# Kernel tuning notes

Measured on AMD Instinct MI355X. Metric: run time of the kernel, lower is better.

Reference implementation:

```python
import jax, jax.numpy as jnp
import numpy as np

B, N, C, H = 2, 2048, 1024, 16
D = C // H  # head_dim = 64


def _rope_freqs(n, d_half, theta=10000.0):
    inv = 1.0 / (theta ** (np.arange(0, d_half, dtype=np.float32) / d_half))
    ang = np.arange(n, dtype=np.float32)[:, None] * inv[None, :]
    return jnp.asarray(np.cos(ang)), jnp.asarray(np.sin(ang))


def setup_inputs() -> dict:
    key = jax.random.key(0)
    ks = jax.random.split(key, 5)
    cos, sin = _rope_freqs(N, D // 2)
    s = 0.02
    return {
        "x": jax.random.normal(ks[0], (B, N, C), jnp.float32),
        "w_qkv": jax.random.normal(ks[1], (3 * C, C), jnp.float32) * s,
        "b_qkv": jnp.zeros((3 * C,), jnp.float32),
        "w_proj": jax.random.normal(ks[2], (C, C), jnp.float32) * s,
        "b_proj": jnp.zeros((C,), jnp.float32),
        "freqs_cos": cos,
        "freqs_sin": sin,
    }


def _apply_rope(t, cos, sin):
    # t: (B, H, N, D); consecutive pairs (even, odd) form complex numbers,
    # matching torch.view_as_complex on reshape(..., D//2, 2).
    te = t[..., 0::2]
    to = t[..., 1::2]
    cos = cos[None, None, :, :]  # (1,1,N,D//2)
    sin = sin[None, None, :, :]
    oe = te * cos - to * sin
    oo = te * sin + to * cos
    return jnp.stack([oe, oo], axis=-1).reshape(t.shape)


def reference(x, w_qkv, b_qkv, w_proj, b_proj, freqs_cos, freqs_sin):
    b, n, c = x.shape
    qkv = x @ w_qkv.T + b_qkv                      # (B,N,3C)
    qkv = qkv.reshape(b, n, 3, H, D).transpose(2, 0, 3, 1, 4)  # (3,B,H,N,D)
    q, k, v = qkv[0], qkv[1], qkv[2]
    q = _apply_rope(q, freqs_cos, freqs_sin)
    k = _apply_rope(k, freqs_cos, freqs_sin)
    scale = 1.0 / jnp.sqrt(jnp.asarray(D, x.dtype))
    scores = jnp.einsum("bhqd,bhkd->bhqk", q, k) * scale
    attn = jax.nn.softmax(scores, axis=-1)
    out = jnp.einsum("bhqk,bhkd->bhqd", attn, v)   # (B,H,N,D)
    out = out.transpose(0, 2, 1, 3).reshape(b, n, c)
    return out @ w_proj.T + b_proj
```

## Files before the change

### kernel.cpp

```cpp
#include <hip/hip_runtime.h>
#include <hip/hip_bf16.h>
#include <stdint.h>

#define BB 2
#define NN 2048
#define CC 1024
#define HH 16
#define DD 64
#define C3 3072

typedef __attribute__((ext_vector_type(8))) short bf16x8;
typedef __attribute__((ext_vector_type(4))) float f32x4;
typedef __attribute__((ext_vector_type(4))) unsigned short ushort4_t;

__device__ __forceinline__ unsigned short f2bf(float f) {
  union { float f; unsigned u; } v; v.f = f;
  unsigned r = v.u + 0x7FFFu + ((v.u >> 16) & 1u);
  return (unsigned short)(r >> 16);
}

#if __has_builtin(__builtin_amdgcn_exp2f)
#define EXP2(x) __builtin_amdgcn_exp2f(x)
#else
#define EXP2(x) exp2f(x)
#endif

#define QSCALE 0.18033688f

#define GLDS(g, l) __builtin_amdgcn_global_load_lds( \
    (const __attribute__((address_space(1))) void*)(g), \
    (__attribute__((address_space(3))) void*)(l), 16, 0, 0)

__global__ __launch_bounds__(256) void k_cvt(
    const float* __restrict__ x, const float* __restrict__ wq,
    const float* __restrict__ wp,
    unsigned short* __restrict__ xb, unsigned short* __restrict__ wqb,
    unsigned short* __restrict__ wpb)
{
  int blk = blockIdx.x;
  const float* s; unsigned short* d; int i;
  if (blk < 4096)      { s = x;  d = xb;  i = blk * 256 + threadIdx.x; }
  else if (blk < 7168) { s = wq; d = wqb; i = (blk - 4096) * 256 + threadIdx.x; }
  else                 { s = wp; d = wpb; i = (blk - 7168) * 256 + threadIdx.x; }
  float4 v = ((const float4*)s)[i];
  ushort4_t o;
  o.x = f2bf(v.x); o.y = f2bf(v.y); o.z = f2bf(v.z); o.w = f2bf(v.w);
  ((ushort4_t*)d)[i] = o;
}

__global__ __launch_bounds__(256) void k_gemm_qkv(
    const unsigned short* __restrict__ A, const unsigned short* __restrict__ Bt,
    const float* __restrict__ bias,
    const float* __restrict__ cosb, const float* __restrict__ sinb,
    unsigned short* __restrict__ Qg, unsigned short* __restrict__ Kg,
    unsigned short* __restrict__ Vnd)
{
  __shared__ __align__(16) unsigned short As[128 * 32];
  __shared__ __align__(16) unsigned short Bs[128 * 32];
  const int tid  = threadIdx.x;
  const int lane = tid & 63;
  const int wave = tid >> 6;
  const int bm = blockIdx.y * 128;
  const int bn = blockIdx.x * 128;
  const int wm = (wave >> 1) * 64;
  const int wn = (wave & 1) * 64;
  const int frow = lane & 15;
  const int fk   = (lane >> 4) * 8;
  const int K = 1024;

  f32x4 acc[4][4] = {};

  const int row0 = tid >> 2, cc0 = tid & 3;
  const int row1 = row0 + 64;

  for (int k0 = 0; k0 < K; k0 += 32) {
    GLDS(A  + (size_t)(bm + row0) * K + k0 + cc0 * 8, As + (size_t)tid * 8);
    GLDS(Bt + (size_t)(bn + row0) * K + k0 + cc0 * 8, Bs + (size_t)tid * 8);
    GLDS(A  + (size_t)(bm + row1) * K + k0 + cc0 * 8, As + (size_t)(tid + 256) * 8);
    GLDS(Bt + (size_t)(bn + row1) * K + k0 + cc0 * 8, Bs + (size_t)(tid + 256) * 8);
    __syncthreads();

    bf16x8 af[4], bfr[4];
#pragma unroll
    for (int t = 0; t < 4; ++t) {
      af[t]  = *(const bf16x8*)(As + (wm + t * 16 + frow) * 32 + fk);
      bfr[t] = *(const bf16x8*)(Bs + (wn + t * 16 + frow) * 32 + fk);
    }
#pragma unroll
    for (int mt = 0; mt < 4; ++mt)
#pragma unroll
      for (int nt = 0; nt < 4; ++nt)
        acc[mt][nt] = __builtin_amdgcn_mfma_f32_16x16x32_bf16(af[mt], bfr[nt], acc[mt][nt], 0, 0, 0);
    __syncthreads();
  }

  const int er0  = (lane >> 4) * 4;
  const int ecol = lane & 15;
  const int region = bn >> 10;
  unsigned short* dstQK = (region == 0) ? Qg : Kg;

#pragma unroll
  for (int nt = 0; nt < 4; ++nt) {
    const int col = bn + wn + nt * 16 + ecol;
    const float bv = bias[col];
    const int c64 = (wn + nt * 16 + ecol) & 63;
    const int h   = (col >> 6) & 15;
    const int ii  = c64 >> 1;
#pragma unroll
    for (int mt = 0; mt < 4; ++mt)
#pragma unroll
      for (int r = 0; r < 4; ++r) {
        const int rowg = bm + wm + mt * 16 + er0 + r;
        const int b = rowg >> 11, n = rowg & (NN - 1);
        float v = acc[mt][nt][r] + bv;
        float vp = __shfl_xor(v, 1, 64);
        const size_t o = ((size_t)(b * HH + h) * NN + n) * DD + c64;
        if (region == 2) {
          Vnd[o] = f2bf(v);
        } else {
          float cth = cosb[n * 32 + ii], sth = sinb[n * 32 + ii];
          float ov = (c64 & 1) ? (vp * sth + v * cth)
                               : (v * cth - vp * sth);
          if (region == 0) ov *= QSCALE;
          dstQK[o] = f2bf(ov);
        }
      }
  }
}

__global__ __launch_bounds__(256) void k_vt(
    const unsigned short* __restrict__ Vnd, unsigned short* __restrict__ Vt)
{
  __shared__ unsigned short t[64][66];
  const int tid = threadIdx.x;
  const int bh = blockIdx.x >> 5;
  const int n0 = (blockIdx.x & 31) * 64;

  const unsigned short* src = Vnd + ((size_t)bh * NN + n0) * DD;
  const int nl = tid >> 2, d0 = (tid & 3) * 16;
#pragma unroll
  for (int j = 0; j < 4; ++j) {
    ushort4_t v = *(const ushort4_t*)(src + (size_t)nl * DD + d0 + j * 4);
    t[nl][d0 + j * 4 + 0] = v.x;
    t[nl][d0 + j * 4 + 1] = v.y;
    t[nl][d0 + j * 4 + 2] = v.z;
    t[nl][d0 + j * 4 + 3] = v.w;
  }
  __syncthreads();
  const int d = tid >> 2, m0 = (tid & 3) * 16;
  unsigned short* dst = Vt + ((size_t)bh * DD + d) * NN + n0 + m0;
#pragma unroll
  for (int j = 0; j < 4; ++j) {
    ushort4_t o;
    o.x = t[m0 + j * 4 + 0][d];
    o.y = t[m0 + j * 4 + 1][d];
    o.z = t[m0 + j * 4 + 2][d];
    o.w = t[m0 + j * 4 + 3][d];
    *(ushort4_t*)(dst + j * 4) = o;
  }
}

__global__ __launch_bounds__(256) void k_attn(
    const unsigned short* __restrict__ Qg, const unsigned short* __restrict__ Kg,
    const unsigned short* __restrict__ Vtg, unsigned short* __restrict__ Og)
{
  __shared__ __align__(16) unsigned short Ks[2][64 * 64];
  __shared__ __align__(16) unsigned short Vs[2][64 * 64];
  __shared__ __align__(16) unsigned short Ps[4][32 * 64];

  const int tid  = threadIdx.x;
  const int lane = tid & 63;
  const int wave = tid >> 6;
  const int bh = blockIdx.x >> 4;
  const int qt = blockIdx.x & 15;
  const int q0 = qt * 128 + wave * 32;
  const int frow   = lane & 15;
  const int fchunk = lane >> 4;
  const int er0  = (lane >> 4) * 4;
  const int ecol = lane & 15;

  const unsigned short* Qb = Qg  + (size_t)bh * NN * DD;
  const unsigned short* Kb = Kg  + (size_t)bh * NN * DD;
  const unsigned short* Vb = Vtg + (size_t)bh * DD * NN;

  bf16x8 qf[2][2];
#pragma unroll
  for (int m = 0; m < 2; ++m)
#pragma unroll
    for (int kt = 0; kt < 2; ++kt)
      qf[m][kt] = *(const bf16x8*)(Qb + (size_t)(q0 + m * 16 + frow) * DD + kt * 32 + fchunk * 8);

  bf16x8 ones;
#pragma unroll
  for (int i = 0; i < 8; ++i) ones[i] = (short)0x3F80;

  f32x4 oacc[2][4] = {};
  f32x4 lacc[2] = {};

  const int row0 = tid >> 3, cc0 = tid & 7;
  const int sw0 = (cc0 ^ (row0 & 7)) * 8;

  GLDS(Kb + (size_t)row0 * DD + sw0,        Ks[0] + (size_t)tid * 8);
  GLDS(Vb + (size_t)row0 * NN + sw0,        Vs[0] + (size_t)tid * 8);
  GLDS(Kb + (size_t)(row0 + 32) * DD + sw0, Ks[0] + (size_t)(tid + 256) * 8);
  GLDS(Vb + (size_t)(row0 + 32) * NN + sw0, Vs[0] + (size_t)(tid + 256) * 8);

  for (int t = 0; t < NN / 64; ++t) {
    const int p = t & 1;
    __syncthreads();

    if (t + 1 < NN / 64) {
      const int j = (t + 1) * 64;
      GLDS(Kb + (size_t)(j + row0) * DD + sw0,      Ks[1 - p] + (size_t)tid * 8);
      GLDS(Vb + (size_t)row0 * NN + j + sw0,        Vs[1 - p] + (size_t)tid * 8);
      GLDS(Kb + (size_t)(j + row0 + 32) * DD + sw0, Ks[1 - p] + (size_t)(tid + 256) * 8);
      GLDS(Vb + (size_t)(row0 + 32) * NN + j + sw0, Vs[1 - p] + (size_t)(tid + 256) * 8);
    }

    f32x4 sacc[2][4] = {};
#pragma unroll
    for (int nt = 0; nt < 4; ++nt) {
      int kr = nt * 16 + frow;
      bf16x8 kf0 = *(const bf16x8*)(Ks[p] + kr * 64 + ((fchunk       ^ (kr & 7)) << 3));
      bf16x8 kf1 = *(const bf16x8*)(Ks[p] + kr * 64 + (((fchunk + 4) ^ (kr & 7)) << 3));
#pragma unroll
      for (int m = 0; m < 2; ++m) {
        sacc[m][nt] = __builtin_amdgcn_mfma_f32_16x16x32_bf16(qf[m][0], kf0, sacc[m][nt], 0, 0, 0);
        sacc[m][nt] = __builtin_amdgcn_mfma_f32_16x16x32_bf16(qf[m][1], kf1, sacc[m][nt], 0, 0, 0);
      }
    }

#pragma unroll
    for (int m = 0; m < 2; ++m)
#pragma unroll
      for (int r = 0; r < 4; ++r) {
        int prow = m * 16 + er0 + r;
#pragma unroll
        for (int nt = 0; nt < 4; ++nt) {
          float pv = EXP2(sacc[m][nt][r]);
          union { float f; unsigned u; } cv; cv.f = pv;
          int col = nt * 16 + ecol;
          Ps[wave][prow * 64 + (((col >> 3) ^ (prow & 7)) << 3) + (col & 7)] =
              (unsigned short)(cv.u >> 16);
        }
      }

    bf16x8 pf0[2], pf1[2];
#pragma unroll
    for (int m = 0; m < 2; ++m) {
      int pr = m * 16 + frow;
      pf0[m] = *(const bf16x8*)(&Ps[wave][pr * 64 + ((fchunk       ^ (pr & 7)) << 3)]);
      pf1[m] = *(const bf16x8*)(&Ps[wave][pr * 64 + (((fchunk + 4) ^ (pr & 7)) << 3)]);
      lacc[m] = __builtin_amdgcn_mfma_f32_16x16x32_bf16(pf0[m], ones, lacc[m], 0, 0, 0);
      lacc[m] = __builtin_amdgcn_mfma_f32_16x16x32_bf16(pf1[m], ones, lacc[m], 0, 0, 0);
    }
#pragma unroll
    for (int dt = 0; dt < 4; ++dt) {
      int vr = dt * 16 + frow;
      bf16x8 vf0 = *(const bf16x8*)(Vs[p] + vr * 64 + ((fchunk       ^ (vr & 7)) << 3));
      bf16x8 vf1 = *(const bf16x8*)(Vs[p] + vr * 64 + (((fchunk + 4) ^ (vr & 7)) << 3));
#pragma unroll
      for (int m = 0; m < 2; ++m) {
        oacc[m][dt] = __builtin_amdgcn_mfma_f32_16x16x32_bf16(pf0[m], vf0, oacc[m][dt], 0, 0, 0);
        oacc[m][dt] = __builtin_amdgcn_mfma_f32_16x16x32_bf16(pf1[m], vf1, oacc[m][dt], 0, 0, 0);
      }
    }
  }

  const int b = bh >> 4;
  const int h = bh & 15;
#pragma unroll
  for (int m = 0; m < 2; ++m)
#pragma unroll
    for (int dt = 0; dt < 4; ++dt)
#pragma unroll
      for (int r = 0; r < 4; ++r) {
        int qrow = q0 + m * 16 + er0 + r;
        int d = dt * 16 + ecol;
        float v = oacc[m][dt][r] / lacc[m][r];
        Og[(size_t)(b * NN + qrow) * CC + h * DD + d] = f2bf(v);
      }
}

__global__ __launch_bounds__(256) void k_gemm_proj(
    const unsigned short* __restrict__ A, const unsigned short* __restrict__ Bt,
    const float* __restrict__ bias, float* __restrict__ Co)
{
  __shared__ __align__(16) unsigned short As[64 * 32];
  __shared__ __align__(16) unsigned short Bs[128 * 32];
  const int tid  = threadIdx.x;
  const int lane = tid & 63;
  const int wave = tid >> 6;
  const int bm = blockIdx.y * 64;
  const int bn = blockIdx.x * 128;
  const int wm = (wave >> 1) * 32;
  const int wn = (wave & 1) * 64;
  const int frow = lane & 15;
  const int fk   = (lane >> 4) * 8;
  const int K = 1024;

  f32x4 acc[2][4] = {};

  const int row0 = tid >> 2, cc0 = tid & 3;

  for (int k0 = 0; k0 < K; k0 += 32) {
    GLDS(A  + (size_t)(bm + row0) * K + k0 + cc0 * 8, As + (size_t)tid * 8);
    GLDS(Bt + (size_t)(bn + row0) * K + k0 + cc0 * 8, Bs + (size_t)tid * 8);
    GLDS(Bt + (size_t)(bn + row0 + 64) * K + k0 + cc0 * 8, Bs + (size_t)(tid + 256) * 8);
    __syncthreads();

    bf16x8 af[2], bfr[4];
#pragma unroll
    for (int t = 0; t < 2; ++t)
      af[t] = *(const bf16x8*)(As + (wm + t * 16 + frow) * 32 + fk);
#pragma unroll
    for (int t = 0; t < 4; ++t)
      bfr[t] = *(const bf16x8*)(Bs + (wn + t * 16 + frow) * 32 + fk);
#pragma unroll
    for (int mt = 0; mt < 2; ++mt)
#pragma unroll
      for (int nt = 0; nt < 4; ++nt)
        acc[mt][nt] = __builtin_amdgcn_mfma_f32_16x16x32_bf16(af[mt], bfr[nt], acc[mt][nt], 0, 0, 0);
    __syncthreads();
  }

  const int er0  = (lane >> 4) * 4;
  const int ecol = lane & 15;
#pragma unroll
  for (int nt = 0; nt < 4; ++nt) {
    int col = bn + wn + nt * 16 + ecol;
    float bv = bias[col];
#pragma unroll
    for (int mt = 0; mt < 2; ++mt)
#pragma unroll
      for (int r = 0; r < 4; ++r) {
        int rowg = bm + wm + mt * 16 + er0 + r;
        Co[(size_t)rowg * CC + col] = acc[mt][nt][r] + bv;
      }
  }
}

extern "C" void kernel_launch(void* const* d_in, const int* in_sizes, int n_in,
                              void* d_out, int out_size, void* d_ws, size_t ws_size,
                              hipStream_t stream)
{
  const float* x      = (const float*)d_in[0];
  const float* w_qkv  = (const float*)d_in[1];
  const float* b_qkv  = (const float*)d_in[2];
  const float* w_proj = (const float*)d_in[3];
  const float* b_proj = (const float*)d_in[4];
  const float* fcos   = (const float*)d_in[5];
  const float* fsin   = (const float*)d_in[6];
  float* out = (float*)d_out;

  char* ws = (char*)d_ws;
  unsigned short* xb     = (unsigned short*)(ws);
  unsigned short* wqkvb  = (unsigned short*)(ws + 8388608);
  unsigned short* wprojb = (unsigned short*)(ws + 14680064);
  unsigned short* Qb     = (unsigned short*)(ws + 16777216);
  unsigned short* Kb     = (unsigned short*)(ws + 25165824);
  unsigned short* Vnd    = (unsigned short*)(ws + 33554432);
  unsigned short* Vtb    = (unsigned short*)(ws + 41943040);
  unsigned short* aob    = (unsigned short*)(ws + 50331648);

  k_cvt<<<8192, 256, 0, stream>>>(x, w_qkv, w_proj, xb, wqkvb, wprojb);

  k_gemm_qkv<<<dim3(24, 32), 256, 0, stream>>>(xb, wqkvb, b_qkv, fcos, fsin,
                                               Qb, Kb, Vnd);
  k_vt<<<1024, 256, 0, stream>>>(Vnd, Vtb);

  k_attn<<<512, 256, 0, stream>>>(Qb, Kb, Vtb, aob);

  k_gemm_proj<<<dim3(8, 64), 256, 0, stream>>>(aob, wprojb, b_proj, out);
}
```

Measured before the change: 226.5 us.

## Split attention over key halves with combine kernel; widen GEMM K-tiles with swizzle

Attention is split across two halves of the key sequence, doubling the block count from 512 to 1024 to fill more compute units. Each half writes unnormalized fp32 partial outputs and row sums, and a new combine kernel adds them, normalizes and emits bf16. Both GEMMs now stage 64-wide K tiles with an XOR-swizzled LDS layout, halving the number of barrier iterations and avoiding bank conflicts. The split adds a kernel launch and about 33 MB of extra fp32 global traffic. Skipping max-subtraction is safe only because partials combine linearly.

```diff
diff --git a/kernel.cpp b/kernel.cpp
--- a/kernel.cpp
+++ b/kernel.cpp
@@ -55,8 +55,8 @@
     unsigned short* __restrict__ Qg, unsigned short* __restrict__ Kg,
     unsigned short* __restrict__ Vnd)
 {
-  __shared__ __align__(16) unsigned short As[128 * 32];
-  __shared__ __align__(16) unsigned short Bs[128 * 32];
+  __shared__ __align__(16) unsigned short As[128 * 64];
+  __shared__ __align__(16) unsigned short Bs[128 * 64];
   const int tid  = threadIdx.x;
   const int lane = tid & 63;
   const int wave = tid >> 6;
@@ -64,33 +64,41 @@
   const int bn = blockIdx.x * 128;
   const int wm = (wave >> 1) * 64;
   const int wn = (wave & 1) * 64;
-  const int frow = lane & 15;
-  const int fk   = (lane >> 4) * 8;
+  const int frow   = lane & 15;
+  const int fchunk = lane >> 4;
   const int K = 1024;
 
   f32x4 acc[4][4] = {};
 
-  const int row0 = tid >> 2, cc0 = tid & 3;
-  const int row1 = row0 + 64;
-
-  for (int k0 = 0; k0 < K; k0 += 32) {
-    GLDS(A  + (size_t)(bm + row0) * K + k0 + cc0 * 8, As + (size_t)tid * 8);
-    GLDS(Bt + (size_t)(bn + row0) * K + k0 + cc0 * 8, Bs + (size_t)tid * 8);
-    GLDS(A  + (size_t)(bm + row1) * K + k0 + cc0 * 8, As + (size_t)(tid + 256) * 8);
-    GLDS(Bt + (size_t)(bn + row1) * K + k0 + cc0 * 8, Bs + (size_t)(tid + 256) * 8);
+  const int srow[4] = { tid >> 3, 32 + (tid >> 3), 64 + (tid >> 3), 96 + (tid >> 3) };
+  int scol[4];
+#pragma unroll
+  for (int j = 0; j < 4; ++j) scol[j] = ((tid & 7) ^ (srow[j] & 7)) * 8;
+
+  for (int k0 = 0; k0 < K; k0 += 64) {
+#pragma unroll
+    for (int j = 0; j < 4; ++j) {
+      GLDS(A  + (size_t)(bm + srow[j]) * K + k0 + scol[j], As + (size_t)(j * 256 + tid) * 8);
+      GLDS(Bt + (size_t)(bn + srow[j]) * K + k0 + scol[j], Bs + (size_t)(j * 256 + tid) * 8);
+    }
     __syncthreads();
 
-    bf16x8 af[4], bfr[4];
-#pragma unroll
-    for (int t = 0; t < 4; ++t) {
-      af[t]  = *(const bf16x8*)(As + (wm + t * 16 + frow) * 32 + fk);
-      bfr[t] = *(const bf16x8*)(Bs + (wn + t * 16 + frow) * 32 + fk);
-    }
-#pragma unroll
-    for (int mt = 0; mt < 4; ++mt)
-#pragma unroll
-      for (int nt = 0; nt < 4; ++nt)
-        acc[mt][nt] = __builtin_amdgcn_mfma_f32_16x16x32_bf16(af[mt], bfr[nt], acc[mt][nt], 0, 0, 0);
+#pragma unroll
+    for (int kh = 0; kh < 2; ++kh) {
+      bf16x8 af[4], bfr[4];
+#pragma unroll
+      for (int t = 0; t < 4; ++t) {
+        int ra = wm + t * 16 + frow;
+        int rb = wn + t * 16 + frow;
+        af[t]  = *(const bf16x8*)(As + ra * 64 + (((kh * 4 + fchunk) ^ (ra & 7)) << 3));
+        bfr[t] = *(const bf16x8*)(Bs + rb * 64 + (((kh * 4 + fchunk) ^ (rb & 7)) << 3));
+      }
+#pragma unroll
+      for (int mt = 0; mt < 4; ++mt)
+#pragma unroll
+        for (int nt = 0; nt < 4; ++nt)
+          acc[mt][nt] = __builtin_amdgcn_mfma_f32_16x16x32_bf16(af[mt], bfr[nt], acc[mt][nt], 0, 0, 0);
+    }
     __syncthreads();
   }
 
@@ -162,17 +170,20 @@
 
 __global__ __launch_bounds__(256) void k_attn(
     const unsigned short* __restrict__ Qg, const unsigned short* __restrict__ Kg,
-    const unsigned short* __restrict__ Vtg, unsigned short* __restrict__ Og)
+    const unsigned short* __restrict__ Vtg,
+    float* __restrict__ Op, float* __restrict__ lp)
 {
   __shared__ __align__(16) unsigned short Ks[2][64 * 64];
   __shared__ __align__(16) unsigned short Vs[2][64 * 64];
-  __shared__ __align__(16) unsigned short Ps[4][32 * 64];
+  __shared__ __align__(16) unsigned short Ps[4][32 * 32];
 
   const int tid  = threadIdx.x;
   const int lane = tid & 63;
   const int wave = tid >> 6;
-  const int bh = blockIdx.x >> 4;
-  const int qt = blockIdx.x & 15;
+  const int blk  = blockIdx.x;
+  const int bh   = blk >> 5;
+  const int qt   = (blk >> 1) & 15;
+  const int half = blk & 1;
   const int q0 = qt * 128 + wave * 32;
   const int frow   = lane & 15;
   const int fchunk = lane >> 4;
@@ -182,6 +193,7 @@
   const unsigned short* Qb = Qg  + (size_t)bh * NN * DD;
   const unsigned short* Kb = Kg  + (size_t)bh * NN * DD;
   const unsigned short* Vb = Vtg + (size_t)bh * DD * NN;
+  const int jbase = half * (NN / 2);
 
   bf16x8 qf[2][2];
 #pragma unroll
@@ -200,17 +212,17 @@
   const int row0 = tid >> 3, cc0 = tid & 7;
   const int sw0 = (cc0 ^ (row0 & 7)) * 8;
 
-  GLDS(Kb + (size_t)row0 * DD + sw0,        Ks[0] + (size_t)tid * 8);
-  GLDS(Vb + (size_t)row0 * NN + sw0,        Vs[0] + (size_t)tid * 8);
-  GLDS(Kb + (size_t)(row0 + 32) * DD + sw0, Ks[0] + (size_t)(tid + 256) * 8);
-  GLDS(Vb + (size_t)(row0 + 32) * NN + sw0, Vs[0] + (size_t)(tid + 256) * 8);
-
-  for (int t = 0; t < NN / 64; ++t) {
+  GLDS(Kb + (size_t)(jbase + row0) * DD + sw0,      Ks[0] + (size_t)tid * 8);
+  GLDS(Vb + (size_t)row0 * NN + jbase + sw0,        Vs[0] + (size_t)tid * 8);
+  GLDS(Kb + (size_t)(jbase + row0 + 32) * DD + sw0, Ks[0] + (size_t)(tid + 256) * 8);
+  GLDS(Vb + (size_t)(row0 + 32) * NN + jbase + sw0, Vs[0] + (size_t)(tid + 256) * 8);
+
+  for (int t = 0; t < NN / 128; ++t) {
     const int p = t & 1;
     __syncthreads();
 
-    if (t + 1 < NN / 64) {
-      const int j = (t + 1) * 64;
+    if (t + 1 < NN / 128) {
+      const int j = jbase + (t + 1) * 64;
       GLDS(Kb + (size_t)(j + row0) * DD + sw0,      Ks[1 - p] + (size_t)tid * 8);
       GLDS(Vb + (size_t)row0 * NN + j + sw0,        Vs[1 - p] + (size_t)tid * 8);
       GLDS(Kb + (size_t)(j + row0 + 32) * DD + sw0, Ks[1 - p] + (size_t)(tid + 256) * 8);
@@ -231,63 +243,87 @@
     }
 
 #pragma unroll
-    for (int m = 0; m < 2; ++m)
-#pragma unroll
-      for (int r = 0; r < 4; ++r) {
-        int prow = m * 16 + er0 + r;
-#pragma unroll
-        for (int nt = 0; nt < 4; ++nt) {
-          float pv = EXP2(sacc[m][nt][r]);
-          union { float f; unsigned u; } cv; cv.f = pv;
-          int col = nt * 16 + ecol;
-          Ps[wave][prow * 64 + (((col >> 3) ^ (prow & 7)) << 3) + (col & 7)] =
-              (unsigned short)(cv.u >> 16);
+    for (int kh = 0; kh < 2; ++kh) {
+#pragma unroll
+      for (int m = 0; m < 2; ++m)
+#pragma unroll
+        for (int r = 0; r < 4; ++r) {
+          int prow = m * 16 + er0 + r;
+#pragma unroll
+          for (int nh = 0; nh < 2; ++nh) {
+            float pv = EXP2(sacc[m][kh * 2 + nh][r]);
+            union { float f; unsigned u; } cv; cv.f = pv;
+            int cl = nh * 16 + ecol;
+            Ps[wave][prow * 32 + (((cl >> 3) ^ (prow & 3)) << 3) + (cl & 7)] =
+                (unsigned short)(cv.u >> 16);
+          }
         }
-      }
-
-    bf16x8 pf0[2], pf1[2];
-#pragma unroll
-    for (int m = 0; m < 2; ++m) {
-      int pr = m * 16 + frow;
-      pf0[m] = *(const bf16x8*)(&Ps[wave][pr * 64 + ((fchunk       ^ (pr & 7)) << 3)]);
-      pf1[m] = *(const bf16x8*)(&Ps[wave][pr * 64 + (((fchunk + 4) ^ (pr & 7)) << 3)]);
-      lacc[m] = __builtin_amdgcn_mfma_f32_16x16x32_bf16(pf0[m], ones, lacc[m], 0, 0, 0);
-      lacc[m] = __builtin_amdgcn_mfma_f32_16x16x32_bf16(pf1[m], ones, lacc[m], 0, 0, 0);
-    }
-#pragma unroll
-    for (int dt = 0; dt < 4; ++dt) {
-      int vr = dt * 16 + frow;
-      bf16x8 vf0 = *(const bf16x8*)(Vs[p] + vr * 64 + ((fchunk       ^ (vr & 7)) << 3));
-      bf16x8 vf1 = *(const bf16x8*)(Vs[p] + vr * 64 + (((fchunk + 4) ^ (vr & 7)) << 3));
+
+      bf16x8 pf[2];
 #pragma unroll
       for (int m = 0; m < 2; ++m) {
-        oacc[m][dt] = __builtin_amdgcn_mfma_f32_16x16x32_bf16(pf0[m], vf0, oacc[m][dt], 0, 0, 0);
-        oacc[m][dt] = __builtin_amdgcn_mfma_f32_16x16x32_bf16(pf1[m], vf1, oacc[m][dt], 0, 0, 0);
-      }
-    }
-  }
-
-  const int b = bh >> 4;
-  const int h = bh & 15;
-#pragma unroll
-  for (int m = 0; m < 2; ++m)
+        int pr = m * 16 + frow;
+        pf[m] = *(const bf16x8*)(&Ps[wave][pr * 32 + ((fchunk ^ (pr & 3)) << 3)]);
+        lacc[m] = __builtin_amdgcn_mfma_f32_16x16x32_bf16(pf[m], ones, lacc[m], 0, 0, 0);
+      }
+#pragma unroll
+      for (int dt = 0; dt < 4; ++dt) {
+        int vr = dt * 16 + frow;
+        bf16x8 vf = *(const bf16x8*)(Vs[p] + vr * 64 + (((kh * 4 + fchunk) ^ (vr & 7)) << 3));
+#pragma unroll
+        for (int m = 0; m < 2; ++m)
+          oacc[m][dt] = __builtin_amdgcn_mfma_f32_16x16x32_bf16(pf[m], vf, oacc[m][dt], 0, 0, 0);
+      }
+    }
+  }
+
+  float* Oh = Op + (size_t)half * (32u * NN * DD);
+#pragma unroll
+  for (int m = 0; m < 2; ++m) {
 #pragma unroll
     for (int dt = 0; dt < 4; ++dt)
 #pragma unroll
       for (int r = 0; r < 4; ++r) {
         int qrow = q0 + m * 16 + er0 + r;
         int d = dt * 16 + ecol;
-        float v = oacc[m][dt][r] / lacc[m][r];
-        Og[(size_t)(b * NN + qrow) * CC + h * DD + d] = f2bf(v);
-      }
+        Oh[((size_t)bh * NN + qrow) * DD + d] = oacc[m][dt][r];
+      }
+    if (ecol == 0) {
+#pragma unroll
+      for (int r = 0; r < 4; ++r) {
+        int qrow = q0 + m * 16 + er0 + r;
+        lp[(size_t)half * (32 * NN) + bh * NN + qrow] = lacc[m][r];
+      }
+    }
+  }
+}
+
+__global__ __launch_bounds__(256) void k_combine(
+    const float* __restrict__ Op, const float* __restrict__ lp,
+    unsigned short* __restrict__ aob)
+{
+  int idx = blockIdx.x * 256 + threadIdx.x;
+  int q  = idx >> 4;
+  int d4 = (idx & 15) * 4;
+  const float4 a = *(const float4*)(Op + (size_t)q * DD + d4);
+  const float4 b = *(const float4*)(Op + (size_t)(32u * NN * DD) + (size_t)q * DD + d4);
+  float inv = 1.0f / (lp[q] + lp[32 * NN + q]);
+  int bh = q >> 11, n = q & (NN - 1);
+  int bb = bh >> 4, h = bh & 15;
+  ushort4_t o;
+  o.x = f2bf((a.x + b.x) * inv);
+  o.y = f2bf((a.y + b.y) * inv);
+  o.z = f2bf((a.z + b.z) * inv);
+  o.w = f2bf((a.w + b.w) * inv);
+  *(ushort4_t*)(aob + ((size_t)(bb * NN + n) * CC) + h * DD + d4) = o;
 }
 
 __global__ __launch_bounds__(256) void k_gemm_proj(
     const unsigned short* __restrict__ A, const unsigned short* __restrict__ Bt,
     const float* __restrict__ bias, float* __restrict__ Co)
 {
-  __shared__ __align__(16) unsigned short As[64 * 32];
-  __shared__ __align__(16) unsigned short Bs[128 * 32];
+  __shared__ __align__(16) unsigned short As[64 * 64];
+  __shared__ __align__(16) unsigned short Bs[128 * 64];
   const int tid  = threadIdx.x;
   const int lane = tid & 63;
   const int wave = tid >> 6;
@@ -295,32 +331,47 @@
   const int bn = blockIdx.x * 128;
   const int wm = (wave >> 1) * 32;
   const int wn = (wave & 1) * 64;
-  const int frow = lane & 15;
-  const int fk   = (lane >> 4) * 8;
+  const int frow   = lane & 15;
+  const int fchunk = lane >> 4;
   const int K = 1024;
 
   f32x4 acc[2][4] = {};
 
-  const int row0 = tid >> 2, cc0 = tid & 3;
-
-  for (int k0 = 0; k0 < K; k0 += 32) {
-    GLDS(A  + (size_t)(bm + row0) * K + k0 + cc0 * 8, As + (size_t)tid * 8);
-    GLDS(Bt + (size_t)(bn + row0) * K + k0 + cc0 * 8, Bs + (size_t)tid * 8);
-    GLDS(Bt + (size_t)(bn + row0 + 64) * K + k0 + cc0 * 8, Bs + (size_t)(tid + 256) * 8);
+  const int r0 = tid >> 3;
+  const int sc0 = ((tid & 7) ^ (r0 & 7)) * 8;
+  const int r1 = 32 + r0;
+  const int sc1 = ((tid & 7) ^ (r1 & 7)) * 8;
+
+  for (int k0 = 0; k0 < K; k0 += 64) {
+    GLDS(A + (size_t)(bm + r0) * K + k0 + sc0, As + (size_t)tid * 8);
+    GLDS(A + (size_t)(bm + r1) * K + k0 + sc1, As + (size_t)(tid + 256) * 8);
+#pragma unroll
+    for (int j = 0; j < 4; ++j) {
+      int rb = j * 32 + r0;
+      int scb = ((tid & 7) ^ (rb & 7)) * 8;
+      GLDS(Bt + (size_t)(bn + rb) * K + k0 + scb, Bs + (size_t)(j * 256 + tid) * 8);
+    }
     __syncthreads();
 
-    bf16x8 af[2], bfr[4];
-#pragma unroll
-    for (int t = 0; t < 2; ++t)
-      af[t] = *(const bf16x8*)(As + (wm + t * 16 + frow) * 32 + fk);
-#pragma unroll
-    for (int t = 0; t < 4; ++t)
-      bfr[t] = *(const bf16x8*)(Bs + (wn + t * 16 + frow) * 32 + fk);
-#pragma unroll
-    for (int mt = 0; mt < 2; ++mt)
-#pragma unroll
-      for (int nt = 0; nt < 4; ++nt)
-        acc[mt][nt] = __builtin_amdgcn_mfma_f32_16x16x32_bf16(af[mt], bfr[nt], acc[mt][nt], 0, 0, 0);
+#pragma unroll
+    for (int kh = 0; kh < 2; ++kh) {
+      bf16x8 af[2], bfr[4];
+#pragma unroll
+      for (int t = 0; t < 2; ++t) {
+        int ra = wm + t * 16 + frow;
+        af[t] = *(const bf16x8*)(As + ra * 64 + (((kh * 4 + fchunk) ^ (ra & 7)) << 3));
+      }
+#pragma unroll
+      for (int t = 0; t < 4; ++t) {
+        int rb = wn + t * 16 + frow;
+        bfr[t] = *(const bf16x8*)(Bs + rb * 64 + (((kh * 4 + fchunk) ^ (rb & 7)) << 3));
+      }
+#pragma unroll
+      for (int mt = 0; mt < 2; ++mt)
+#pragma unroll
+        for (int nt = 0; nt < 4; ++nt)
+          acc[mt][nt] = __builtin_amdgcn_mfma_f32_16x16x32_bf16(af[mt], bfr[nt], acc[mt][nt], 0, 0, 0);
+    }
     __syncthreads();
   }
 
@@ -362,6 +413,8 @@
   unsigned short* Vnd    = (unsigned short*)(ws + 33554432);
   unsigned short* Vtb    = (unsigned short*)(ws + 41943040);
   unsigned short* aob    = (unsigned short*)(ws + 50331648);
+  float*          Op     = (float*)(ws + 58720256);
+  float*          lp     = (float*)(ws + 92274688);
 
   k_cvt<<<8192, 256, 0, stream>>>(x, w_qkv, w_proj, xb, wqkvb, wprojb);
 
@@ -369,7 +422,8 @@
                                                Qb, Kb, Vnd);
   k_vt<<<1024, 256, 0, stream>>>(Vnd, Vtb);
 
-  k_attn<<<512, 256, 0, stream>>>(Qb, Kb, Vtb, aob);
+  k_attn<<<1024, 256, 0, stream>>>(Qb, Kb, Vtb, Op, lp);
+  k_combine<<<4096, 256, 0, stream>>>(Op, lp, aob);
 
   k_gemm_proj<<<dim3(8, 64), 256, 0, stream>>>(aob, wprojb, b_proj, out);
 }
```

Measured after the change: 237.7 us. 1.05x slower.
